# Kernel optimization log

Measured on AMD Instinct MI355X. Metric: run time of the kernel, lower is better.

The kernel has to match this reference:

```python
import jax, jax.numpy as jnp
import numpy as np

B, N, C = 8, 512, 64
VOCAB = 200000
TEMP = 0.07
THR = 0.99
EPS = 1e-8


def _norm(x):
    # torch F.normalize: x / clamp(||x||, min=eps)
    return x / jnp.maximum(jnp.linalg.norm(x, axis=-1, keepdims=True), EPS)


def setup_inputs() -> dict:
    key = jax.random.key(0)
    k = jax.random.split(key, 6)
    return {
        "Q": jax.random.normal(k[0], (B, N, C), dtype=jnp.float32),
        "Pos": jax.random.normal(k[1], (B, N, C), dtype=jnp.float32),
        "neg_global": jax.random.normal(k[2], (B, N, C), dtype=jnp.float32),
        "pos_item_ids": jax.random.randint(k[3], (B, N), 0, VOCAB),
        "neg_global_item_ids": jax.random.randint(k[4], (B, N), 0, VOCAB),
        "log_q_table": jax.random.normal(k[5], (VOCAB,), dtype=jnp.float32),
    }


def reference(Q, Pos, neg_global, pos_item_ids, neg_global_item_ids, log_q_table):
    B_, N_, C_ = Q.shape
    BN = B_ * N_
    Qn, Pn, Gn = _norm(Q), _norm(Pos), _norm(neg_global)
    Qf = Qn.reshape(BN, C_)
    Pf = Pn.reshape(BN, C_)
    Nf = Gn.reshape(BN, C_)
    pos_ids = pos_item_ids.reshape(BN)
    neg_ids = neg_global_item_ids.reshape(BN)
    row_seq = jnp.arange(BN) // N_  # sequence index of each flattened row
    neg_inf = jnp.float32(-jnp.inf)

    # ---- global negatives ----
    p2n = (Pf @ Nf.T).reshape(B_, N_, BN)            # (B, N, BN) cosine Pos vs neg
    ok_glob = (jnp.max(p2n, axis=1) <= THR)[row_seq]  # (BN, BN) per-seq max mask
    sim_glob = (Qf @ Nf.T) / TEMP
    logits_glob = jnp.where(ok_glob, sim_glob - log_q_table[neg_ids][None, :], neg_inf)

    # ---- in-batch negatives ----
    p2p = (Pf @ Pf.T).reshape(B_, N_, BN)
    diff_seq = row_seq[:, None] != row_seq[None, :]
    ok_ibn = (jnp.max(p2p, axis=1) <= THR)[row_seq] & diff_seq
    sim_ibn = (Qf @ Pf.T) / TEMP
    logits_ibn = jnp.where(ok_ibn, sim_ibn - log_q_table[pos_ids][None, :], neg_inf)

    # ---- positive logits ----
    pos_logits = (jnp.sum(Qn * Pn, axis=-1) / TEMP).reshape(BN, 1)
    pos_logits = pos_logits - log_q_table[pos_ids][:, None]

    # concat: (BN, 1 + 2*BN)
    return jnp.concatenate([pos_logits, logits_glob, logits_ibn], axis=1)
```

## Files before the change

kernel.cpp:

```cpp
#include <hip/hip_runtime.h>
#include <math.h>

#define B_  8
#define N_  512
#define C_  64
#define BN  4096
#define OUTW 8193
#define INV_TEMP 14.285714285714286f
#define THR_ 0.99f
#define NEG_HUGE -1e30f

typedef __attribute__((ext_vector_type(8))) short short8v;
typedef __attribute__((ext_vector_type(4))) float f32x4;

#define WSB_QN   0
#define WSB_PN   (512*1024)
#define WSB_GN   (1024*1024)
#define WSB_LQP  (1536*1024)
#define WSB_LQN  (WSB_LQP + 16*1024)
#define WSB_MAXG (WSB_LQP + 32*1024)
#define WSB_MAXI (WSB_MAXG + 128*1024)

__device__ __forceinline__ unsigned short f2bf(float f) {
  unsigned u = __float_as_uint(f);
  u += 0x7fffu + ((u >> 16) & 1u);
  return (unsigned short)(u >> 16);
}

__device__ __forceinline__ void load_lds16(const void* g, void* l) {
  __builtin_amdgcn_global_load_lds(
      (const __attribute__((address_space(1))) unsigned int*)g,
      (__attribute__((address_space(3))) unsigned int*)l, 16, 0, 0);
}

__global__ __launch_bounds__(256) void kprep(const float* __restrict__ Q,
    const float* __restrict__ P, const float* __restrict__ G,
    const int* __restrict__ pos_ids, const int* __restrict__ neg_ids,
    const float* __restrict__ table, unsigned short* __restrict__ wbf,
    float* __restrict__ lqp, float* __restrict__ lqn, float* __restrict__ out) {
  int gw   = blockIdx.x * 4 + (threadIdx.x >> 6);
  int lane = threadIdx.x & 63;
  int t = gw >> 12, r = gw & 4095;
  const float* src = (t == 0) ? Q : (t == 1 ? P : G);
  float x = src[(size_t)r * C_ + lane];
  float s = x * x;
  #pragma unroll
  for (int off = 32; off; off >>= 1) s += __shfl_xor(s, off);
  float inv = 1.0f / fmaxf(sqrtf(s), 1e-8f);
  wbf[(size_t)t * BN * C_ + (size_t)r * C_ + lane] = f2bf(x * inv);

  if (t == 0) {
    float p = P[(size_t)r * C_ + lane];
    float pp = p * p, qp = x * p;
    #pragma unroll
    for (int off = 32; off; off >>= 1) {
      pp += __shfl_xor(pp, off);
      qp += __shfl_xor(qp, off);
    }
    if (lane == 0) {
      float d = qp / (fmaxf(sqrtf(s), 1e-8f) * fmaxf(sqrtf(pp), 1e-8f));
      float lp = table[pos_ids[r]];
      out[(size_t)r * OUTW] = d * INV_TEMP - lp;
      lqp[r] = lp;
      lqn[r] = table[neg_ids[r]];
    }
  }
}

__global__ __launch_bounds__(256) void kmaskM(const unsigned short* __restrict__ PN,
    const unsigned short* __restrict__ GN, float* __restrict__ maxout) {
  __shared__ uint4 B4[1024];
  __shared__ uint4 A4[2][1024];
  __shared__ float red[2][128];
  int tid = threadIdx.x;
  int jt = blockIdx.x, b = blockIdx.y, z = blockIdx.z;
  const unsigned short* X = z ? PN : GN;
  int j0 = jt * 128;

  #pragma unroll
  for (int it = 0; it < 4; ++it) {
    int idx = tid + 256 * it, row = idx >> 3, kc = idx & 7;
    load_lds16(X + (size_t)(j0 + row) * C_ + (kc ^ (row & 7)) * 8, &B4[idx]);
    load_lds16(PN + (size_t)(b * N_ + row) * C_ + (kc ^ (row & 7)) * 8,
               &A4[0][idx]);
  }
  int wid = tid >> 6, lane = tid & 63;
  int m0 = (wid >> 1) * 64, n0 = (wid & 1) * 64;
  int lr = lane & 15, lk = lane >> 4;
  const short8v* Bs = (const short8v*)B4;
  float mcol[4] = {NEG_HUGE, NEG_HUGE, NEG_HUGE, NEG_HUGE};

  for (int ch = 0; ch < 4; ++ch) {
    __syncthreads();
    if (ch < 3) {
      #pragma unroll
      for (int it = 0; it < 4; ++it) {
        int idx = tid + 256 * it, row = idx >> 3, kc = idx & 7;
        load_lds16(PN + (size_t)(b * N_ + (ch + 1) * 128 + row) * C_ +
                       (kc ^ (row & 7)) * 8,
                   &A4[(ch + 1) & 1][idx]);
      }
    }
    const short8v* As = (const short8v*)A4[ch & 1];

    f32x4 zz = {0.f, 0.f, 0.f, 0.f};
    f32x4 acc[4][4];
    #pragma unroll
    for (int mf = 0; mf < 4; ++mf)
      #pragma unroll
      for (int nf = 0; nf < 4; ++nf) acc[mf][nf] = zz;

    #pragma unroll
    for (int ks = 0; ks < 2; ++ks) {
      int kc = lk + ks * 4;
      short8v a[4], bgs[4];
      #pragma unroll
      for (int mf = 0; mf < 4; ++mf) {
        int r = m0 + mf * 16 + lr;
        a[mf] = As[r * 8 + (kc ^ (r & 7))];
      }
      #pragma unroll
      for (int nf = 0; nf < 4; ++nf) {
        int r = n0 + nf * 16 + lr;
        bgs[nf] = Bs[r * 8 + (kc ^ (r & 7))];
      }
      #pragma unroll
      for (int mf = 0; mf < 4; ++mf)
        #pragma unroll
        for (int nf = 0; nf < 4; ++nf)
          acc[mf][nf] = __builtin_amdgcn_mfma_f32_16x16x32_bf16(
              a[mf], bgs[nf], acc[mf][nf], 0, 0, 0);
    }
    #pragma unroll
    for (int nf = 0; nf < 4; ++nf)
      #pragma unroll
      for (int mf = 0; mf < 4; ++mf)
        #pragma unroll
        for (int rg = 0; rg < 4; ++rg)
          mcol[nf] = fmaxf(mcol[nf], acc[mf][nf][rg]);
  }
  #pragma unroll
  for (int nf = 0; nf < 4; ++nf) {
    float v = mcol[nf];
    v = fmaxf(v, __shfl_xor(v, 16));
    v = fmaxf(v, __shfl_xor(v, 32));
    mcol[nf] = v;
  }
  int wn = wid >> 1, wj = wid & 1;
  if (lane < 16) {
    #pragma unroll
    for (int nf = 0; nf < 4; ++nf)
      red[wn][wj * 64 + nf * 16 + lane] = mcol[nf];
  }
  __syncthreads();
  if (tid < 128)
    maxout[(size_t)(z * 8 + b) * 4096 + j0 + tid] =
        fmaxf(red[0][tid], red[1][tid]);
}

__global__ __launch_bounds__(256) void klogitsM(const unsigned short* __restrict__ QN,
    const unsigned short* __restrict__ PN, const unsigned short* __restrict__ GN,
    const float* __restrict__ lqp, const float* __restrict__ lqn,
    const float* __restrict__ maxg, const float* __restrict__ maxi,
    float* __restrict__ out) {
  __shared__ uint4 AB4[2048];
  __shared__ float oks[128];
  __shared__ float lqs[128];
  int tid = threadIdx.x;
  int jt = blockIdx.y, half = jt >> 5;
  int j0 = (jt & 31) * 128;
  int i0 = blockIdx.x * 128;
  size_t colbase = 1 + (size_t)half * BN + j0;

  if (half && ((i0 >> 9) == (j0 >> 9))) {
    f32x4 nh = {NEG_HUGE, NEG_HUGE, NEG_HUGE, NEG_HUGE};
    #pragma unroll
    for (int it = 0; it < 16; ++it) {
      int idx = tid + 256 * it;
      int row = idx >> 5, c4 = (idx & 31) * 4;
      *(f32x4*)(out + (size_t)(i0 + row) * OUTW + colbase + c4) = nh;
    }
    return;
  }

  const unsigned short* X = half ? PN : GN;
  const float* lq = half ? lqp : lqn;
  const float* mc = (half ? maxi : maxg) + (size_t)(i0 >> 9) * 4096;

  if (tid < 128) {
    oks[tid] = (mc[j0 + tid] <= THR_) ? 1.0f : 0.0f;
    lqs[tid] = lq[j0 + tid];
  }
  #pragma unroll
  for (int it = 0; it < 4; ++it) {
    int idx = tid + 256 * it, row = idx >> 3, kc = idx & 7;
    int sc = (kc ^ (row & 7)) * 8;
    load_lds16(QN + (size_t)(i0 + row) * C_ + sc, &AB4[idx]);
    load_lds16(X  + (size_t)(j0 + row) * C_ + sc, &AB4[1024 + idx]);
  }
  __syncthreads();

  int wid = tid >> 6, lane = tid & 63;
  int lr = lane & 15, lk = lane >> 4;
  const short8v* As = (const short8v*)AB4;
  const short8v* Bs = (const short8v*)(AB4 + 1024);

  f32x4 zz = {0.f, 0.f, 0.f, 0.f};
  f32x4 acc[2][8];
  #pragma unroll
  for (int mh = 0; mh < 2; ++mh)
    #pragma unroll
    for (int nf = 0; nf < 8; ++nf) acc[mh][nf] = zz;

  #pragma unroll
  for (int ks = 0; ks < 2; ++ks) {
    int kc = lk + ks * 4;
    short8v a2[2], bb[8];
    #pragma unroll
    for (int mh = 0; mh < 2; ++mh) {
      int r = mh * 64 + wid * 16 + lr;
      a2[mh] = As[r * 8 + (kc ^ (r & 7))];
    }
    #pragma unroll
    for (int nf = 0; nf < 8; ++nf) {
      int r = nf * 16 + lr;
      bb[nf] = Bs[r * 8 + (kc ^ (r & 7))];
    }
    #pragma unroll
    for (int mh = 0; mh < 2; ++mh)
      #pragma unroll
      for (int nf = 0; nf < 8; ++nf)
        acc[mh][nf] = __builtin_amdgcn_mfma_f32_16x16x32_bf16(
            a2[mh], bb[nf], acc[mh][nf], 0, 0, 0);
  }

  float* stage = (float*)AB4;
  #pragma unroll
  for (int h = 0; h < 2; ++h) {
    __syncthreads();
    #pragma unroll
    for (int nf = 0; nf < 8; ++nf) {
      int j = nf * 16 + lr;
      float okv = oks[j];
      float lqv = lqs[j];
      #pragma unroll
      for (int rg = 0; rg < 4; ++rg) {
        int rowh = wid * 16 + lk * 4 + rg;
        float v = acc[h][nf][rg] * INV_TEMP - lqv;
        v = (okv != 0.0f) ? v : NEG_HUGE;
        int cq = (j >> 2) ^ ((rowh >> 2) & 7);
        stage[rowh * 128 + cq * 4 + (j & 3)] = v;
      }
    }
    __syncthreads();
    #pragma unroll
    for (int it = 0; it < 8; ++it) {
      int idx = tid + 256 * it;
      int row = idx >> 5, q = idx & 31;
      int cq = q ^ ((row >> 2) & 7);
      f32x4 v = *(const f32x4*)(stage + row * 128 + cq * 4);
      *(f32x4*)(out + (size_t)(i0 + h * 64 + row) * OUTW + colbase + q * 4) = v;
    }
  }
}

extern "C" void kernel_launch(void* const* d_in, const int* in_sizes, int n_in,
                              void* d_out, int out_size, void* d_ws, size_t ws_size,
                              hipStream_t stream) {
  const float* Q = (const float*)d_in[0];
  const float* P = (const float*)d_in[1];
  const float* G = (const float*)d_in[2];
  const int* pos_ids = (const int*)d_in[3];
  const int* neg_ids = (const int*)d_in[4];
  const float* table = (const float*)d_in[5];
  float* out = (float*)d_out;
  char* w = (char*)d_ws;
  unsigned short* QN = (unsigned short*)(w + WSB_QN);
  unsigned short* PN = (unsigned short*)(w + WSB_PN);
  unsigned short* GN = (unsigned short*)(w + WSB_GN);
  float* LQP = (float*)(w + WSB_LQP);
  float* LQN = (float*)(w + WSB_LQN);
  float* MAXG = (float*)(w + WSB_MAXG);
  float* MAXI = (float*)(w + WSB_MAXI);

  kprep<<<dim3(3 * BN / 4), 256, 0, stream>>>(Q, P, G, pos_ids, neg_ids, table,
                                              QN, LQP, LQN, out);
  kmaskM<<<dim3(32, 8, 2), 256, 0, stream>>>(PN, GN, MAXG);
  klogitsM<<<dim3(32, 64), 256, 0, stream>>>(QN, PN, GN, LQP, LQN,
                                             MAXG, MAXI, out);
}
```

Before: 161.8 us.

## Fuse three kernels into one persistent cooperative kernel with grid syncs

Replaces the prep, mask-max and logits launches with a single cooperative kernel of 512 blocks. Grid-wide barriers separate the phases, and the shared memory is unioned across them. This removes two kernel launches and the gaps between them. In exchange, the logits phase now runs 4 tasks per block serially instead of 2048 independent blocks, and it adds the cost of grid-wide synchronization.

```diff
diff --git a/kernel.cpp b/kernel.cpp
--- a/kernel.cpp
+++ b/kernel.cpp
@@ -1,5 +1,8 @@
 #include <hip/hip_runtime.h>
+#include <hip/hip_cooperative_groups.h>
 #include <math.h>
+
+namespace cg = cooperative_groups;
 
 #define B_  8
 #define N_  512
@@ -19,7 +22,6 @@
 #define WSB_LQP  (1536*1024)
 #define WSB_LQN  (WSB_LQP + 16*1024)
 #define WSB_MAXG (WSB_LQP + 32*1024)
-#define WSB_MAXI (WSB_MAXG + 128*1024)
 
 __device__ __forceinline__ unsigned short f2bf(float f) {
   unsigned u = __float_as_uint(f);
@@ -33,233 +35,245 @@
       (__attribute__((address_space(3))) unsigned int*)l, 16, 0, 0);
 }
 
-__global__ __launch_bounds__(256) void kprep(const float* __restrict__ Q,
+struct P2S { uint4 B4[1024]; uint4 A4[2][1024]; float red[2][128]; };
+struct P3S { uint4 AB4[2048]; float oks[128]; float lqs[128]; };
+union SMEMU { P2S p2; P3S p3; };
+
+__global__ __launch_bounds__(256) void kfused(const float* __restrict__ Q,
     const float* __restrict__ P, const float* __restrict__ G,
     const int* __restrict__ pos_ids, const int* __restrict__ neg_ids,
     const float* __restrict__ table, unsigned short* __restrict__ wbf,
-    float* __restrict__ lqp, float* __restrict__ lqn, float* __restrict__ out) {
-  int gw   = blockIdx.x * 4 + (threadIdx.x >> 6);
-  int lane = threadIdx.x & 63;
-  int t = gw >> 12, r = gw & 4095;
-  const float* src = (t == 0) ? Q : (t == 1 ? P : G);
-  float x = src[(size_t)r * C_ + lane];
-  float s = x * x;
-  #pragma unroll
-  for (int off = 32; off; off >>= 1) s += __shfl_xor(s, off);
-  float inv = 1.0f / fmaxf(sqrtf(s), 1e-8f);
-  wbf[(size_t)t * BN * C_ + (size_t)r * C_ + lane] = f2bf(x * inv);
-
-  if (t == 0) {
-    float p = P[(size_t)r * C_ + lane];
-    float pp = p * p, qp = x * p;
-    #pragma unroll
-    for (int off = 32; off; off >>= 1) {
-      pp += __shfl_xor(pp, off);
-      qp += __shfl_xor(qp, off);
-    }
-    if (lane == 0) {
-      float d = qp / (fmaxf(sqrtf(s), 1e-8f) * fmaxf(sqrtf(pp), 1e-8f));
-      float lp = table[pos_ids[r]];
-      out[(size_t)r * OUTW] = d * INV_TEMP - lp;
-      lqp[r] = lp;
-      lqn[r] = table[neg_ids[r]];
+    float* __restrict__ lqp, float* __restrict__ lqn,
+    float* __restrict__ maxout, float* __restrict__ out) {
+  cg::grid_group gridg = cg::this_grid();
+  __shared__ SMEMU sm;
+  int tid = threadIdx.x;
+  int blk = blockIdx.x;
+  int wid = tid >> 6, lane = tid & 63;
+  int lr = lane & 15, lk = lane >> 4;
+  const unsigned short* PN = wbf + (size_t)BN * C_;
+  const unsigned short* GN = wbf + (size_t)2 * BN * C_;
+
+  {
+    int wave_global = blk * 4 + wid;
+    #pragma unroll
+    for (int k = 0; k < 6; ++k) {
+      int gw = wave_global + 2048 * k;
+      int t = gw >> 12, r = gw & 4095;
+      const float* src = (t == 0) ? Q : (t == 1 ? P : G);
+      float x = src[(size_t)r * C_ + lane];
+      float s = x * x;
+      #pragma unroll
+      for (int off = 32; off; off >>= 1) s += __shfl_xor(s, off);
+      float inv = 1.0f / fmaxf(sqrtf(s), 1e-8f);
+      wbf[(size_t)t * BN * C_ + (size_t)r * C_ + lane] = f2bf(x * inv);
+
+      if (t == 0) {
+        float p = P[(size_t)r * C_ + lane];
+        float pp = p * p, qp = x * p;
+        #pragma unroll
+        for (int off = 32; off; off >>= 1) {
+          pp += __shfl_xor(pp, off);
+          qp += __shfl_xor(qp, off);
+        }
+        if (lane == 0) {
+          float d = qp / (fmaxf(sqrtf(s), 1e-8f) * fmaxf(sqrtf(pp), 1e-8f));
+          float lp = table[pos_ids[r]];
+          out[(size_t)r * OUTW] = d * INV_TEMP - lp;
+          lqp[r] = lp;
+          lqn[r] = table[neg_ids[r]];
+        }
+      }
     }
   }
-}
-
-__global__ __launch_bounds__(256) void kmaskM(const unsigned short* __restrict__ PN,
-    const unsigned short* __restrict__ GN, float* __restrict__ maxout) {
-  __shared__ uint4 B4[1024];
-  __shared__ uint4 A4[2][1024];
-  __shared__ float red[2][128];
-  int tid = threadIdx.x;
-  int jt = blockIdx.x, b = blockIdx.y, z = blockIdx.z;
-  const unsigned short* X = z ? PN : GN;
-  int j0 = jt * 128;
-
-  #pragma unroll
-  for (int it = 0; it < 4; ++it) {
-    int idx = tid + 256 * it, row = idx >> 3, kc = idx & 7;
-    load_lds16(X + (size_t)(j0 + row) * C_ + (kc ^ (row & 7)) * 8, &B4[idx]);
-    load_lds16(PN + (size_t)(b * N_ + row) * C_ + (kc ^ (row & 7)) * 8,
-               &A4[0][idx]);
+  __threadfence();
+  gridg.sync();
+
+  {
+    int jt = blk & 31, b = (blk >> 5) & 7, z = blk >> 8;
+    const unsigned short* X = z ? PN : GN;
+    int j0 = jt * 128;
+
+    #pragma unroll
+    for (int it = 0; it < 4; ++it) {
+      int idx = tid + 256 * it, row = idx >> 3, kc = idx & 7;
+      load_lds16(X + (size_t)(j0 + row) * C_ + (kc ^ (row & 7)) * 8,
+                 &sm.p2.B4[idx]);
+      load_lds16(PN + (size_t)(b * N_ + row) * C_ + (kc ^ (row & 7)) * 8,
+                 &sm.p2.A4[0][idx]);
+    }
+    int m0 = (wid >> 1) * 64, n0 = (wid & 1) * 64;
+    const short8v* Bs = (const short8v*)sm.p2.B4;
+    float mcol[4] = {NEG_HUGE, NEG_HUGE, NEG_HUGE, NEG_HUGE};
+
+    for (int ch = 0; ch < 4; ++ch) {
+      __syncthreads();
+      if (ch < 3) {
+        #pragma unroll
+        for (int it = 0; it < 4; ++it) {
+          int idx = tid + 256 * it, row = idx >> 3, kc = idx & 7;
+          load_lds16(PN + (size_t)(b * N_ + (ch + 1) * 128 + row) * C_ +
+                         (kc ^ (row & 7)) * 8,
+                     &sm.p2.A4[(ch + 1) & 1][idx]);
+        }
+      }
+      const short8v* As = (const short8v*)sm.p2.A4[ch & 1];
+
+      f32x4 zz = {0.f, 0.f, 0.f, 0.f};
+      f32x4 acc[4][4];
+      #pragma unroll
+      for (int mf = 0; mf < 4; ++mf)
+        #pragma unroll
+        for (int nf = 0; nf < 4; ++nf) acc[mf][nf] = zz;
+
+      #pragma unroll
+      for (int ks = 0; ks < 2; ++ks) {
+        int kc = lk + ks * 4;
+        short8v a[4], bgs[4];
+        #pragma unroll
+        for (int mf = 0; mf < 4; ++mf) {
+          int r = m0 + mf * 16 + lr;
+          a[mf] = As[r * 8 + (kc ^ (r & 7))];
+        }
+        #pragma unroll
+        for (int nf = 0; nf < 4; ++nf) {
+          int r = n0 + nf * 16 + lr;
+          bgs[nf] = Bs[r * 8 + (kc ^ (r & 7))];
+        }
+        #pragma unroll
+        for (int mf = 0; mf < 4; ++mf)
+          #pragma unroll
+          for (int nf = 0; nf < 4; ++nf)
+            acc[mf][nf] = __builtin_amdgcn_mfma_f32_16x16x32_bf16(
+                a[mf], bgs[nf], acc[mf][nf], 0, 0, 0);
+      }
+      #pragma unroll
+      for (int nf = 0; nf < 4; ++nf)
+        #pragma unroll
+        for (int mf = 0; mf < 4; ++mf)
+          #pragma unroll
+          for (int rg = 0; rg < 4; ++rg)
+            mcol[nf] = fmaxf(mcol[nf], acc[mf][nf][rg]);
+    }
+    #pragma unroll
+    for (int nf = 0; nf < 4; ++nf) {
+      float v = mcol[nf];
+      v = fmaxf(v, __shfl_xor(v, 16));
+      v = fmaxf(v, __shfl_xor(v, 32));
+      mcol[nf] = v;
+    }
+    int wn = wid >> 1, wj = wid & 1;
+    if (lane < 16) {
+      #pragma unroll
+      for (int nf = 0; nf < 4; ++nf)
+        sm.p2.red[wn][wj * 64 + nf * 16 + lane] = mcol[nf];
+    }
+    __syncthreads();
+    if (tid < 128)
+      maxout[(size_t)(z * 8 + b) * 4096 + j0 + tid] =
+          fmaxf(sm.p2.red[0][tid], sm.p2.red[1][tid]);
   }
-  int wid = tid >> 6, lane = tid & 63;
-  int m0 = (wid >> 1) * 64, n0 = (wid & 1) * 64;
-  int lr = lane & 15, lk = lane >> 4;
-  const short8v* Bs = (const short8v*)B4;
-  float mcol[4] = {NEG_HUGE, NEG_HUGE, NEG_HUGE, NEG_HUGE};
-
-  for (int ch = 0; ch < 4; ++ch) {
+  __threadfence();
+  gridg.sync();
+
+  const float* maxg = maxout;
+  const float* maxi = maxout + 8 * 4096;
+  for (int k2 = 0; k2 < 4; ++k2) {
+    int task = blk + 512 * k2;
+    int i0 = (task & 31) * 128;
+    int jt = task >> 5, half = jt >> 5;
+    int j0 = (jt & 31) * 128;
+    size_t colbase = 1 + (size_t)half * BN + j0;
+
     __syncthreads();
-    if (ch < 3) {
-      #pragma unroll
-      for (int it = 0; it < 4; ++it) {
-        int idx = tid + 256 * it, row = idx >> 3, kc = idx & 7;
-        load_lds16(PN + (size_t)(b * N_ + (ch + 1) * 128 + row) * C_ +
-                       (kc ^ (row & 7)) * 8,
-                   &A4[(ch + 1) & 1][idx]);
-      }
-    }
-    const short8v* As = (const short8v*)A4[ch & 1];
+
+    if (half && ((i0 >> 9) == (j0 >> 9))) {
+      f32x4 nh = {NEG_HUGE, NEG_HUGE, NEG_HUGE, NEG_HUGE};
+      #pragma unroll
+      for (int it = 0; it < 16; ++it) {
+        int idx = tid + 256 * it;
+        int row = idx >> 5, c4 = (idx & 31) * 4;
+        *(f32x4*)(out + (size_t)(i0 + row) * OUTW + colbase + c4) = nh;
+      }
+      continue;
+    }
+
+    const unsigned short* X = half ? PN : wbf + (size_t)2 * BN * C_;
+    const float* lq = half ? lqp : lqn;
+    const float* mc = (half ? maxi : maxg) + (size_t)(i0 >> 9) * 4096;
+
+    if (tid < 128) {
+      sm.p3.oks[tid] = (mc[j0 + tid] <= THR_) ? 1.0f : 0.0f;
+      sm.p3.lqs[tid] = lq[j0 + tid];
+    }
+    #pragma unroll
+    for (int it = 0; it < 4; ++it) {
+      int idx = tid + 256 * it, row = idx >> 3, kc = idx & 7;
+      int sc = (kc ^ (row & 7)) * 8;
+      load_lds16(wbf + (size_t)(i0 + row) * C_ + sc, &sm.p3.AB4[idx]);
+      load_lds16(X   + (size_t)(j0 + row) * C_ + sc, &sm.p3.AB4[1024 + idx]);
+    }
+    __syncthreads();
+
+    const short8v* As = (const short8v*)sm.p3.AB4;
+    const short8v* Bs = (const short8v*)(sm.p3.AB4 + 1024);
 
     f32x4 zz = {0.f, 0.f, 0.f, 0.f};
-    f32x4 acc[4][4];
-    #pragma unroll
-    for (int mf = 0; mf < 4; ++mf)
-      #pragma unroll
-      for (int nf = 0; nf < 4; ++nf) acc[mf][nf] = zz;
+    f32x4 acc[2][8];
+    #pragma unroll
+    for (int mh = 0; mh < 2; ++mh)
+      #pragma unroll
+      for (int nf = 0; nf < 8; ++nf) acc[mh][nf] = zz;
 
     #pragma unroll
     for (int ks = 0; ks < 2; ++ks) {
       int kc = lk + ks * 4;
-      short8v a[4], bgs[4];
-      #pragma unroll
-      for (int mf = 0; mf < 4; ++mf) {
-        int r = m0 + mf * 16 + lr;
-        a[mf] = As[r * 8 + (kc ^ (r & 7))];
-      }
-      #pragma unroll
-      for (int nf = 0; nf < 4; ++nf) {
-        int r = n0 + nf * 16 + lr;
-        bgs[nf] = Bs[r * 8 + (kc ^ (r & 7))];
-      }
-      #pragma unroll
-      for (int mf = 0; mf < 4; ++mf)
-        #pragma unroll
-        for (int nf = 0; nf < 4; ++nf)
-          acc[mf][nf] = __builtin_amdgcn_mfma_f32_16x16x32_bf16(
-              a[mf], bgs[nf], acc[mf][nf], 0, 0, 0);
-    }
-    #pragma unroll
-    for (int nf = 0; nf < 4; ++nf)
-      #pragma unroll
-      for (int mf = 0; mf < 4; ++mf)
-        #pragma unroll
-        for (int rg = 0; rg < 4; ++rg)
-          mcol[nf] = fmaxf(mcol[nf], acc[mf][nf][rg]);
-  }
-  #pragma unroll
-  for (int nf = 0; nf < 4; ++nf) {
-    float v = mcol[nf];
-    v = fmaxf(v, __shfl_xor(v, 16));
-    v = fmaxf(v, __shfl_xor(v, 32));
-    mcol[nf] = v;
-  }
-  int wn = wid >> 1, wj = wid & 1;
-  if (lane < 16) {
-    #pragma unroll
-    for (int nf = 0; nf < 4; ++nf)
-      red[wn][wj * 64 + nf * 16 + lane] = mcol[nf];
-  }
-  __syncthreads();
-  if (tid < 128)
-    maxout[(size_t)(z * 8 + b) * 4096 + j0 + tid] =
-        fmaxf(red[0][tid], red[1][tid]);
-}
-
-__global__ __launch_bounds__(256) void klogitsM(const unsigned short* __restrict__ QN,
-    const unsigned short* __restrict__ PN, const unsigned short* __restrict__ GN,
-    const float* __restrict__ lqp, const float* __restrict__ lqn,
-    const float* __restrict__ maxg, const float* __restrict__ maxi,
-    float* __restrict__ out) {
-  __shared__ uint4 AB4[2048];
-  __shared__ float oks[128];
-  __shared__ float lqs[128];
-  int tid = threadIdx.x;
-  int jt = blockIdx.y, half = jt >> 5;
-  int j0 = (jt & 31) * 128;
-  int i0 = blockIdx.x * 128;
-  size_t colbase = 1 + (size_t)half * BN + j0;
-
-  if (half && ((i0 >> 9) == (j0 >> 9))) {
-    f32x4 nh = {NEG_HUGE, NEG_HUGE, NEG_HUGE, NEG_HUGE};
-    #pragma unroll
-    for (int it = 0; it < 16; ++it) {
-      int idx = tid + 256 * it;
-      int row = idx >> 5, c4 = (idx & 31) * 4;
-      *(f32x4*)(out + (size_t)(i0 + row) * OUTW + colbase + c4) = nh;
-    }
-    return;
-  }
-
-  const unsigned short* X = half ? PN : GN;
-  const float* lq = half ? lqp : lqn;
-  const float* mc = (half ? maxi : maxg) + (size_t)(i0 >> 9) * 4096;
-
-  if (tid < 128) {
-    oks[tid] = (mc[j0 + tid] <= THR_) ? 1.0f : 0.0f;
-    lqs[tid] = lq[j0 + tid];
-  }
-  #pragma unroll
-  for (int it = 0; it < 4; ++it) {
-    int idx = tid + 256 * it, row = idx >> 3, kc = idx & 7;
-    int sc = (kc ^ (row & 7)) * 8;
-    load_lds16(QN + (size_t)(i0 + row) * C_ + sc, &AB4[idx]);
-    load_lds16(X  + (size_t)(j0 + row) * C_ + sc, &AB4[1024 + idx]);
-  }
-  __syncthreads();
-
-  int wid = tid >> 6, lane = tid & 63;
-  int lr = lane & 15, lk = lane >> 4;
-  const short8v* As = (const short8v*)AB4;
-  const short8v* Bs = (const short8v*)(AB4 + 1024);
-
-  f32x4 zz = {0.f, 0.f, 0.f, 0.f};
-  f32x4 acc[2][8];
-  #pragma unroll
-  for (int mh = 0; mh < 2; ++mh)
-    #pragma unroll
-    for (int nf = 0; nf < 8; ++nf) acc[mh][nf] = zz;
-
-  #pragma unroll
-  for (int ks = 0; ks < 2; ++ks) {
-    int kc = lk + ks * 4;
-    short8v a2[2], bb[8];
-    #pragma unroll
-    for (int mh = 0; mh < 2; ++mh) {
-      int r = mh * 64 + wid * 16 + lr;
-      a2[mh] = As[r * 8 + (kc ^ (r & 7))];
-    }
-    #pragma unroll
-    for (int nf = 0; nf < 8; ++nf) {
-      int r = nf * 16 + lr;
-      bb[nf] = Bs[r * 8 + (kc ^ (r & 7))];
-    }
-    #pragma unroll
-    for (int mh = 0; mh < 2; ++mh)
-      #pragma unroll
-      for (int nf = 0; nf < 8; ++nf)
-        acc[mh][nf] = __builtin_amdgcn_mfma_f32_16x16x32_bf16(
-            a2[mh], bb[nf], acc[mh][nf], 0, 0, 0);
-  }
-
-  float* stage = (float*)AB4;
-  #pragma unroll
-  for (int h = 0; h < 2; ++h) {
-    __syncthreads();
-    #pragma unroll
-    for (int nf = 0; nf < 8; ++nf) {
-      int j = nf * 16 + lr;
-      float okv = oks[j];
-      float lqv = lqs[j];
-      #pragma unroll
-      for (int rg = 0; rg < 4; ++rg) {
-        int rowh = wid * 16 + lk * 4 + rg;
-        float v = acc[h][nf][rg] * INV_TEMP - lqv;
-        v = (okv != 0.0f) ? v : NEG_HUGE;
-        int cq = (j >> 2) ^ ((rowh >> 2) & 7);
-        stage[rowh * 128 + cq * 4 + (j & 3)] = v;
-      }
-    }
-    __syncthreads();
-    #pragma unroll
-    for (int it = 0; it < 8; ++it) {
-      int idx = tid + 256 * it;
-      int row = idx >> 5, q = idx & 31;
-      int cq = q ^ ((row >> 2) & 7);
-      f32x4 v = *(const f32x4*)(stage + row * 128 + cq * 4);
-      *(f32x4*)(out + (size_t)(i0 + h * 64 + row) * OUTW + colbase + q * 4) = v;
+      short8v a2[2], bb[8];
+      #pragma unroll
+      for (int mh = 0; mh < 2; ++mh) {
+        int r = mh * 64 + wid * 16 + lr;
+        a2[mh] = As[r * 8 + (kc ^ (r & 7))];
+      }
+      #pragma unroll
+      for (int nf = 0; nf < 8; ++nf) {
+        int r = nf * 16 + lr;
+        bb[nf] = Bs[r * 8 + (kc ^ (r & 7))];
+      }
+      #pragma unroll
+      for (int mh = 0; mh < 2; ++mh)
+        #pragma unroll
+        for (int nf = 0; nf < 8; ++nf)
+          acc[mh][nf] = __builtin_amdgcn_mfma_f32_16x16x32_bf16(
+              a2[mh], bb[nf], acc[mh][nf], 0, 0, 0);
+    }
+
+    float* stage = (float*)sm.p3.AB4;
+    #pragma unroll
+    for (int h = 0; h < 2; ++h) {
+      __syncthreads();
+      #pragma unroll
+      for (int nf = 0; nf < 8; ++nf) {
+        int j = nf * 16 + lr;
+        float okv = sm.p3.oks[j];
+        float lqv = sm.p3.lqs[j];
+        #pragma unroll
+        for (int rg = 0; rg < 4; ++rg) {
+          int rowh = wid * 16 + lk * 4 + rg;
+          float v = acc[h][nf][rg] * INV_TEMP - lqv;
+          v = (okv != 0.0f) ? v : NEG_HUGE;
+          int cq = (j >> 2) ^ ((rowh >> 2) & 7);
+          stage[rowh * 128 + cq * 4 + (j & 3)] = v;
+        }
+      }
+      __syncthreads();
+      #pragma unroll
+      for (int it = 0; it < 8; ++it) {
+        int idx = tid + 256 * it;
+        int row = idx >> 5, q = idx & 31;
+        int cq = q ^ ((row >> 2) & 7);
+        f32x4 v = *(const f32x4*)(stage + row * 128 + cq * 4);
+        *(f32x4*)(out + (size_t)(i0 + h * 64 + row) * OUTW + colbase + q * 4) = v;
+      }
     }
   }
 }
@@ -275,17 +289,14 @@
   const float* table = (const float*)d_in[5];
   float* out = (float*)d_out;
   char* w = (char*)d_ws;
-  unsigned short* QN = (unsigned short*)(w + WSB_QN);
-  unsigned short* PN = (unsigned short*)(w + WSB_PN);
-  unsigned short* GN = (unsigned short*)(w + WSB_GN);
+  unsigned short* WBF = (unsigned short*)(w + WSB_QN);
   float* LQP = (float*)(w + WSB_LQP);
   float* LQN = (float*)(w + WSB_LQN);
   float* MAXG = (float*)(w + WSB_MAXG);
-  float* MAXI = (float*)(w + WSB_MAXI);
-
-  kprep<<<dim3(3 * BN / 4), 256, 0, stream>>>(Q, P, G, pos_ids, neg_ids, table,
-                                              QN, LQP, LQN, out);
-  kmaskM<<<dim3(32, 8, 2), 256, 0, stream>>>(PN, GN, MAXG);
-  klogitsM<<<dim3(32, 64), 256, 0, stream>>>(QN, PN, GN, LQP, LQN,
-                                             MAXG, MAXI, out);
+
+  void* args[] = {(void*)&Q, (void*)&P, (void*)&G, (void*)&pos_ids,
+                  (void*)&neg_ids, (void*)&table, (void*)&WBF, (void*)&LQP,
+                  (void*)&LQN, (void*)&MAXG, (void*)&out};
+  hipLaunchCooperativeKernel((void*)kfused, dim3(512), dim3(256), args, 0,
+                             stream);
 }
```

Measured after the change: 361.5 us. 2.23x slower.
